# Performance work log

Measured on AMD Instinct MI355X. Metric: run time of the kernel, lower is better.

## Reference

```python
import jax, jax.numpy as jnp
import numpy as np

EPS = 1e-5
NUM_HEAD = 8
HEAD_DIM = 64
SCALE = HEAD_DIM ** -0.5


def setup_inputs() -> dict:
    key = jax.random.key(0)
    ks = jax.random.split(key, 3)
    b, n, dim = 4, 2048, 512
    inner = NUM_HEAD * HEAD_DIM  # 512
    x = jax.random.normal(ks[0], (b, n, dim), dtype=jnp.float32)
    ln_w = jnp.ones((dim,), jnp.float32)
    ln_b = jnp.zeros((dim,), jnp.float32)
    qkv_w = jax.random.normal(ks[1], (3 * inner, dim), jnp.float32) * (dim ** -0.5)
    qkv_b = jnp.zeros((3 * inner,), jnp.float32)
    out_w = jax.random.normal(ks[2], (dim, inner), jnp.float32) * (inner ** -0.5)
    out_b = jnp.zeros((dim,), jnp.float32)
    return {"x": x, "ln_w": ln_w, "ln_b": ln_b, "qkv_w": qkv_w,
            "qkv_b": qkv_b, "out_w": out_w, "out_b": out_b}


def reference(x, ln_w, ln_b, qkv_w, qkv_b, out_w, out_b):
    b, n, dim = x.shape
    # Pre-norm LayerNorm
    mu = jnp.mean(x, axis=-1, keepdims=True)
    var = jnp.mean(jnp.square(x - mu), axis=-1, keepdims=True)
    xn = (x - mu) * jax.lax.rsqrt(var + EPS) * ln_w + ln_b
    # QKV projection (torch Linear: y = x @ W.T + b)
    qkv = xn @ qkv_w.T + qkv_b  # [b, n, 3*inner]
    q, k, v = jnp.split(qkv, 3, axis=-1)
    def heads(t):  # [b, n, inner] -> [b, h, n, d]
        return t.reshape(b, n, NUM_HEAD, HEAD_DIM).transpose(0, 2, 1, 3)
    q, k, v = heads(q), heads(k), heads(v)
    # Naive full attention (materializes [b, h, n, n])
    dots = jnp.einsum('bhqd,bhkd->bhqk', q, k) * SCALE
    attn = jax.nn.softmax(dots, axis=-1)
    o = jnp.einsum('bhqk,bhkd->bhqd', attn, v)
    o = o.transpose(0, 2, 1, 3).reshape(b, n, NUM_HEAD * HEAD_DIM)
    return o @ out_w.T + out_b
```

## Files before the change

### kernel.cpp

```cpp
#include <hip/hip_runtime.h>

typedef __attribute__((ext_vector_type(8))) short bf16x8;
typedef __attribute__((ext_vector_type(4))) float floatx4;
typedef __attribute__((ext_vector_type(16))) float floatx16;
typedef __attribute__((ext_vector_type(4))) unsigned int uintx4;

#define B_    4
#define N_    2048
#define DIM_  512
#define NH_   8
#define HD_   64
#define SCALE_ 0.125f
#define SL2E_ (0.125f * 1.44269504f)

__device__ __forceinline__ unsigned short f32_to_bf16(float f) {
    return (unsigned short)((__float_as_uint(f) + 0x8000u) >> 16);
}

__device__ __forceinline__ float bf16_to_f32(unsigned short u) {
    return __uint_as_float(((unsigned int)u) << 16);
}

__device__ __forceinline__ floatx4 mfma16(bf16x8 a, bf16x8 b, floatx4 c) {
    return __builtin_amdgcn_mfma_f32_16x16x32_bf16(a, b, c, 0, 0, 0);
}

__device__ __forceinline__ floatx16 mfma32(bf16x8 a, bf16x8 b, floatx16 c) {
    return __builtin_amdgcn_mfma_f32_32x32x16_bf16(a, b, c, 0, 0, 0);
}

__device__ __forceinline__ floatx4 fzero4() {
    floatx4 z = {0.f, 0.f, 0.f, 0.f};
    return z;
}

__device__ __forceinline__ floatx16 fzero16() {
    floatx16 z;
#pragma unroll
    for (int i = 0; i < 16; i++) z[i] = 0.f;
    return z;
}

__device__ __forceinline__ unsigned int cvt_pk_bf16(float lo, float hi) {
    unsigned int r;
    asm("v_cvt_pk_bf16_f32 %0, %1, %2" : "=v"(r) : "v"(lo), "v"(hi));
    return r;
}

__device__ __forceinline__ void async16(const unsigned short* g, unsigned short* l) {
    __builtin_amdgcn_global_load_lds((const __attribute__((address_space(1))) void*)g,
                                     (__attribute__((address_space(3))) void*)l,
                                     16, 0, 0);
}

__global__ __launch_bounds__(256) void ln_kernel(const float* __restrict__ x,
                                                 const float* __restrict__ w,
                                                 const float* __restrict__ b,
                                                 unsigned short* __restrict__ xn) {
    int wv = threadIdx.x >> 6;
    int lane = threadIdx.x & 63;
    int row = blockIdx.x * 4 + wv;
    const float4* xr = (const float4*)(x + (size_t)row * DIM_);
    float4 v0 = xr[lane * 2];
    float4 v1 = xr[lane * 2 + 1];
    float s  = (v0.x + v0.y + v0.z + v0.w) + (v1.x + v1.y + v1.z + v1.w);
    float sq = v0.x*v0.x + v0.y*v0.y + v0.z*v0.z + v0.w*v0.w +
               v1.x*v1.x + v1.y*v1.y + v1.z*v1.z + v1.w*v1.w;
#pragma unroll
    for (int off = 1; off < 64; off <<= 1) {
        s  += __shfl_xor(s, off, 64);
        sq += __shfl_xor(sq, off, 64);
    }
    float mu   = s * (1.f / DIM_);
    float var  = sq * (1.f / DIM_) - mu * mu;
    float rstd = rsqrtf(var + 1e-5f);
    float4 w0 = ((const float4*)w)[lane * 2];
    float4 w1 = ((const float4*)w)[lane * 2 + 1];
    float4 b0 = ((const float4*)b)[lane * 2];
    float4 b1 = ((const float4*)b)[lane * 2 + 1];
    float y[8];
    y[0] = (v0.x - mu) * rstd * w0.x + b0.x;
    y[1] = (v0.y - mu) * rstd * w0.y + b0.y;
    y[2] = (v0.z - mu) * rstd * w0.z + b0.z;
    y[3] = (v0.w - mu) * rstd * w0.w + b0.w;
    y[4] = (v1.x - mu) * rstd * w1.x + b1.x;
    y[5] = (v1.y - mu) * rstd * w1.y + b1.y;
    y[6] = (v1.z - mu) * rstd * w1.z + b1.z;
    y[7] = (v1.w - mu) * rstd * w1.w + b1.w;
    uint4 pk;
    pk.x = (unsigned int)f32_to_bf16(y[0]) | ((unsigned int)f32_to_bf16(y[1]) << 16);
    pk.y = (unsigned int)f32_to_bf16(y[2]) | ((unsigned int)f32_to_bf16(y[3]) << 16);
    pk.z = (unsigned int)f32_to_bf16(y[4]) | ((unsigned int)f32_to_bf16(y[5]) << 16);
    pk.w = (unsigned int)f32_to_bf16(y[6]) | ((unsigned int)f32_to_bf16(y[7]) << 16);
    ((uint4*)(xn + (size_t)row * DIM_))[lane] = pk;
}

__global__ __launch_bounds__(256) void cvt_kernel(const float* __restrict__ srcA, int na,
                                                  const float* __restrict__ srcB, int nb,
                                                  unsigned short* __restrict__ dstA,
                                                  unsigned short* __restrict__ dstB) {
    int idx = blockIdx.x * 256 + threadIdx.x;
    if (idx < na)            dstA[idx] = f32_to_bf16(srcA[idx]);
    else if (idx < na + nb)  dstB[idx - na] = f32_to_bf16(srcB[idx - na]);
}

#define GEMM_CORE512(A_, B_ptr, am0, bn0)                                           \
    __shared__ unsigned short Alds[2][128][32];                                     \
    __shared__ unsigned short Blds[2][128][32];                                     \
    int tid = threadIdx.x, lane = tid & 63, wid = tid >> 6;                         \
    int l15 = lane & 15, quad = lane >> 4;                                          \
    int wmloc = (wid >> 1) * 32, wnloc = (wid & 1) * 64;                            \
    int sr = lane >> 2;                                                             \
    int sc = (lane & 3) * 8;                                                        \
    int srow0 = 16 * wid;                                                           \
    floatx4 acc[2][4];                                                              \
    _Pragma("unroll")                                                               \
    for (int i = 0; i < 2; i++)                                                     \
        _Pragma("unroll")                                                           \
        for (int j = 0; j < 4; j++) acc[i][j] = fzero4();                           \
    int buf = 0;                                                                    \
    async16(A_ + (size_t)(am0 + srow0 + sr) * DIM_ + sc, &Alds[0][srow0][0]);       \
    async16(B_ptr + (size_t)(bn0 + srow0 + sr) * DIM_ + sc, &Blds[0][srow0][0]);    \
    __syncthreads();                                                                \
    for (int t = 0; t < 16; t++) {                                                  \
        if (t < 15) {                                                               \
            int k0 = (t + 1) * 32;                                                  \
            async16(A_ + (size_t)(am0 + srow0 + sr) * DIM_ + k0 + sc,               \
                    &Alds[buf ^ 1][srow0][0]);                                      \
            async16(B_ptr + (size_t)(bn0 + srow0 + sr) * DIM_ + k0 + sc,            \
                    &Blds[buf ^ 1][srow0][0]);                                      \
        }                                                                           \
        bf16x8 av[2], bv[4];                                                        \
        _Pragma("unroll")                                                           \
        for (int i = 0; i < 2; i++)                                                 \
            av[i] = *(const bf16x8*)(&Alds[buf][wmloc + 16 * i + l15][quad * 8]);   \
        _Pragma("unroll")                                                           \
        for (int j = 0; j < 4; j++)                                                 \
            bv[j] = *(const bf16x8*)(&Blds[buf][wnloc + 16 * j + l15][quad * 8]);   \
        _Pragma("unroll")                                                           \
        for (int i = 0; i < 2; i++)                                                 \
            _Pragma("unroll")                                                       \
            for (int j = 0; j < 4; j++)                                             \
                acc[i][j] = mfma16(av[i], bv[j], acc[i][j]);                        \
        __syncthreads();                                                            \
        buf ^= 1;                                                                   \
    }

__global__ __launch_bounds__(512, 4) void qkv_gemm(const unsigned short* __restrict__ A,
                                                   const unsigned short* __restrict__ Bw,
                                                   const float* __restrict__ bias,
                                                   unsigned short* __restrict__ Qh,
                                                   unsigned short* __restrict__ Kh,
                                                   unsigned short* __restrict__ Vt) {
    int am0 = blockIdx.x * 128, bn0 = blockIdx.y * 128;
    GEMM_CORE512(A, Bw, am0, bn0)

    if (bn0 >= 1024) {
        unsigned short* sc_ = &Alds[0][0][0] + wid * (16 * 40);
        int m0 = am0 + wmloc;
        int bidx = m0 >> 11;
        int t0 = m0 & 2047;
#pragma unroll
        for (int j = 0; j < 4; j++) {
            float bias_n = bias[bn0 + wnloc + 16 * j + l15];
#pragma unroll
            for (int i = 0; i < 2; i++)
#pragma unroll
                for (int r = 0; r < 4; r++)
                    sc_[l15 * 40 + 16 * i + quad * 4 + r] =
                        f32_to_bf16(acc[i][j][r] + bias_n);
            int nr = lane >> 2;
            int rem = (bn0 - 1024) + wnloc + 16 * j + nr;
            int head = rem >> 6, d = rem & 63;
            bf16x8 vv = *(const bf16x8*)(sc_ + nr * 40 + (lane & 3) * 8);
            *(bf16x8*)(Vt + ((size_t)(bidx * NH_ + head) * HD_ + d) * N_ +
                       t0 + (lane & 3) * 8) = vv;
        }
    } else {
#pragma unroll
        for (int i = 0; i < 2; i++) {
#pragma unroll
            for (int j = 0; j < 4; j++) {
                int n = bn0 + wnloc + 16 * j + l15;
                float bias_n = bias[n];
                int which = n >> 9;
                int rem = n & 511;
                int head = rem >> 6;
                int d = rem & 63;
#pragma unroll
                for (int r = 0; r < 4; r++) {
                    int m = am0 + wmloc + 16 * i + quad * 4 + r;
                    int b = m >> 11;
                    int t = m & 2047;
                    float val = acc[i][j][r] + bias_n;
                    if (which == 0) {
                        Qh[((size_t)(b * NH_ + head) * N_ + t) * HD_ + d] =
                            f32_to_bf16(val * SL2E_);
                    } else {
                        Kh[((size_t)(b * NH_ + head) * N_ + t) * HD_ + d] =
                            f32_to_bf16(val);
                    }
                }
            }
        }
    }
}

__global__ __launch_bounds__(256, 4) void out_gemm_fused(const unsigned short* __restrict__ Opart,
                                                         const float* __restrict__ lpart,
                                                         const unsigned short* __restrict__ Bw,
                                                         const float* __restrict__ bias,
                                                         float* __restrict__ out) {
    __shared__ unsigned short Alds[2][64][36];
    __shared__ unsigned short Blds[2][128][32];
    int tid = threadIdx.x, lane = tid & 63, wid = tid >> 6;
    int l15 = lane & 15, quad = lane >> 4;
    int wmloc = (wid >> 1) * 32, wnloc = (wid & 1) * 64;
    int am0 = blockIdx.x * 64, bn0 = blockIdx.y * 128;

    int arow = tid >> 2;
    int ac8 = (tid & 3) * 8;
    int token = am0 + arow;
    int bb = token >> 11;
    const size_t LSTR = (size_t)B_ * NH_ * N_;
    const size_t OSTR = (size_t)B_ * N_ * DIM_;
    const unsigned short* arow0 = Opart + (size_t)token * DIM_;
    const unsigned short* arow1 = arow0 + OSTR;

    int sr = lane >> 2;
    int sc = (lane & 3) * 8;

    floatx4 acc[2][4];
#pragma unroll
    for (int i = 0; i < 2; i++)
#pragma unroll
        for (int j = 0; j < 4; j++) acc[i][j] = fzero4();

#define STAGE_A(BUF, T)                                                         \
    {                                                                           \
        int k0 = (T) * 32;                                                      \
        int head = k0 >> 6;                                                     \
        size_t li = (size_t)(bb * NH_ + head) * N_ + (token & 2047);            \
        float l1 = lpart[li];                                                   \
        float l2 = lpart[LSTR + li];                                            \
        float inv = 1.f / (l1 + l2);                                            \
        float w1 = l1 * inv, w2 = l2 * inv;                                     \
        bf16x8 o0 = *(const bf16x8*)(arow0 + k0 + ac8);                         \
        bf16x8 o1 = *(const bf16x8*)(arow1 + k0 + ac8);                         \
        bf16x8 pk;                                                              \
        _Pragma("unroll")                                                       \
        for (int e = 0; e < 8; e++)                                             \
            pk[e] = (short)f32_to_bf16(                                         \
                w1 * bf16_to_f32((unsigned short)o0[e]) +                       \
                w2 * bf16_to_f32((unsigned short)o1[e]));                       \
        *(bf16x8*)(&Alds[BUF][arow][ac8]) = pk;                                 \
    }

#define STAGE_B(BUF, T)                                                         \
    {                                                                           \
        int k0 = (T) * 32;                                                      \
        _Pragma("unroll")                                                       \
        for (int i = 0; i < 2; i++) {                                           \
            int r0 = 32 * wid + 16 * i;                                         \
            async16(Bw + (size_t)(bn0 + r0 + sr) * DIM_ + k0 + sc,              \
                    &Blds[BUF][r0][0]);                                         \
        }                                                                       \
    }

    STAGE_B(0, 0)
    STAGE_A(0, 0)
    __syncthreads();
    int buf = 0;
    for (int t = 0; t < 16; t++) {
        if (t < 15) {
            STAGE_B(buf ^ 1, t + 1)
            STAGE_A(buf ^ 1, t + 1)
        }
        bf16x8 av[2], bv[4];
#pragma unroll
        for (int i = 0; i < 2; i++)
            av[i] = *(const bf16x8*)(&Alds[buf][wmloc + 16 * i + l15][quad * 8]);
#pragma unroll
        for (int j = 0; j < 4; j++)
            bv[j] = *(const bf16x8*)(&Blds[buf][wnloc + 16 * j + l15][quad * 8]);
#pragma unroll
        for (int i = 0; i < 2; i++)
#pragma unroll
            for (int j = 0; j < 4; j++)
                acc[i][j] = mfma16(av[i], bv[j], acc[i][j]);
        __syncthreads();
        buf ^= 1;
    }
#undef STAGE_A
#undef STAGE_B

#pragma unroll
    for (int i = 0; i < 2; i++) {
#pragma unroll
        for (int j = 0; j < 4; j++) {
            int n = bn0 + wnloc + 16 * j + l15;
            float bias_n = bias[n];
#pragma unroll
            for (int r = 0; r < 4; r++) {
                int m = am0 + wmloc + 16 * i + quad * 4 + r;
                out[(size_t)m * DIM_ + n] = acc[i][j][r] + bias_n;
            }
        }
    }
}

__global__ __launch_bounds__(256, 4) void attn_kernel(const unsigned short* __restrict__ Qh,
                                                      const unsigned short* __restrict__ Kh,
                                                      const unsigned short* __restrict__ Vtg,
                                                      unsigned short* __restrict__ Opart,
                                                      float* __restrict__ lpart) {
    int bh = blockIdx.y;
    int b = bh >> 3, head = bh & 7;
    int qt = blockIdx.x;
    int split = blockIdx.z;
    int kv0 = split << 10;
    int tid = threadIdx.x, lane = tid & 63, w = tid >> 6;
    int l31 = lane & 31, hi = lane >> 5;
    int xr = l31 & 7;

    const unsigned short* Qp = Qh + (size_t)bh * N_ * HD_;
    const unsigned short* Kg = Kh + (size_t)bh * N_ * HD_;
    const unsigned short* Vg = Vtg + (size_t)bh * HD_ * N_;

    int q0 = qt * 128 + w * 32;

    bf16x8 aQ[4];
    {
        const unsigned short* qrow = Qp + (size_t)(q0 + l31) * HD_ + hi * 8;
#pragma unroll
        for (int t = 0; t < 4; t++)
            aQ[t] = *(const bf16x8*)(qrow + 16 * t);
    }

    __shared__ unsigned short Kt[2][64][64];
    __shared__ unsigned short Vs[2][64][64];
    __shared__ float l_sm[4][32];

    int srow = lane >> 3;
    int scol = ((lane & 7) ^ srow) * 8;

#define STAGE_KV(BUF, KV)                                                           \
    {                                                                               \
        _Pragma("unroll")                                                           \
        for (int i = 0; i < 2; i++) {                                               \
            int r0 = 16 * w + 8 * i;                                                \
            async16(Kg + (size_t)((KV) + r0 + srow) * HD_ + scol, &Kt[BUF][r0][0]); \
            async16(Vg + (size_t)(r0 + srow) * N_ + (KV) + scol, &Vs[BUF][r0][0]);  \
        }                                                                           \
    }

    STAGE_KV(0, kv0)
    __syncthreads();

    floatx16 of[2];
    of[0] = fzero16();
    of[1] = fzero16();
    float lsumA = 0.f, lsumB = 0.f;

    int buf = 0;
    for (int it = 0; it < 16; it++) {
        if (it < 15) {
            STAGE_KV(buf ^ 1, kv0 + (it + 1) * 64)
        }
        bf16x8 pa[4];
#pragma unroll
        for (int tau = 0; tau < 2; tau++) {
            bf16x8 kf[4];
#pragma unroll
            for (int t = 0; t < 4; t++)
                kf[t] = *(const bf16x8*)(&Kt[buf][32 * tau + l31][((2 * t + hi) ^ xr) * 8]);
            floatx16 acc = fzero16();
            __builtin_amdgcn_s_setprio(1);
#pragma unroll
            for (int t = 0; t < 4; t++)
                acc = mfma32(kf[t], aQ[t], acc);
            __builtin_amdgcn_s_setprio(0);
            float p[16];
#pragma unroll
            for (int r = 0; r < 16; r += 2) {
                p[r]     = exp2f(acc[r]);
                p[r + 1] = exp2f(acc[r + 1]);
                lsumA += p[r];
                lsumB += p[r + 1];
            }
            unsigned int a0 = cvt_pk_bf16(p[0], p[1]);
            unsigned int b0 = cvt_pk_bf16(p[4], p[5]);
            unsigned int a1 = cvt_pk_bf16(p[2], p[3]);
            unsigned int b1 = cvt_pk_bf16(p[6], p[7]);
            unsigned int a2 = cvt_pk_bf16(p[8], p[9]);
            unsigned int b2 = cvt_pk_bf16(p[12], p[13]);
            unsigned int a3 = cvt_pk_bf16(p[10], p[11]);
            unsigned int b3 = cvt_pk_bf16(p[14], p[15]);
            asm("v_permlane32_swap_b32 %0, %1" : "+v"(a0), "+v"(b0));
            asm("v_permlane32_swap_b32 %0, %1" : "+v"(a1), "+v"(b1));
            asm("v_permlane32_swap_b32 %0, %1" : "+v"(a2), "+v"(b2));
            asm("v_permlane32_swap_b32 %0, %1" : "+v"(a3), "+v"(b3));
            uintx4 f0 = {a0, a1, b0, b1};
            uintx4 f1 = {a2, a3, b2, b3};
            pa[2 * tau]     = __builtin_bit_cast(bf16x8, f0);
            pa[2 * tau + 1] = __builtin_bit_cast(bf16x8, f1);
        }
        __builtin_amdgcn_s_setprio(1);
#pragma unroll
        for (int s = 0; s < 4; s++) {
#pragma unroll
            for (int dt = 0; dt < 2; dt++) {
                bf16x8 vf = *(const bf16x8*)(&Vs[buf][32 * dt + l31][((2 * s + hi) ^ xr) * 8]);
                of[dt] = mfma32(pa[s], vf, of[dt]);
            }
        }
        __builtin_amdgcn_s_setprio(0);
        __syncthreads();
        buf ^= 1;
    }
#undef STAGE_KV

    float lsum = lsumA + lsumB;
    lsum += __shfl_xor(lsum, 32, 64);
    if (lane < 32) {
        l_sm[w][l31] = 1.f / lsum;
        lpart[(size_t)split * B_ * NH_ * N_ + (size_t)bh * N_ + q0 + l31] = lsum;
    }
    __syncthreads();

    unsigned short* Od = Opart + (size_t)split * B_ * N_ * DIM_;
#pragma unroll
    for (int r = 0; r < 16; r++) {
        int qr = (r & 3) + 8 * (r >> 2) + 4 * hi;
        float inv = l_sm[w][qr];
        int token = q0 + qr;
        size_t base = ((size_t)b * N_ + token) * DIM_ + (size_t)head * HD_;
#pragma unroll
        for (int dt = 0; dt < 2; dt++)
            Od[base + 32 * dt + l31] = f32_to_bf16(of[dt][r] * inv);
    }
}

extern "C" void kernel_launch(void* const* d_in, const int* in_sizes, int n_in,
                              void* d_out, int out_size, void* d_ws, size_t ws_size,
                              hipStream_t stream) {
    const float* x     = (const float*)d_in[0];
    const float* ln_w  = (const float*)d_in[1];
    const float* ln_b  = (const float*)d_in[2];
    const float* qkv_w = (const float*)d_in[3];
    const float* qkv_b = (const float*)d_in[4];
    const float* out_w = (const float*)d_in[5];
    const float* out_b = (const float*)d_in[6];
    float* out = (float*)d_out;

    char* ws = (char*)d_ws;
    const size_t TOK = (size_t)B_ * N_;
    unsigned short* xn    = (unsigned short*)ws;  ws += TOK * DIM_ * 2;
    unsigned short* wq_bf = (unsigned short*)ws;  ws += (size_t)3 * DIM_ * DIM_ * 2;
    unsigned short* wo_bf = (unsigned short*)ws;  ws += (size_t)DIM_ * DIM_ * 2;
    unsigned short* Qh    = (unsigned short*)ws;  ws += TOK * DIM_ * 2;
    unsigned short* Kh    = (unsigned short*)ws;  ws += TOK * DIM_ * 2;
    unsigned short* Vt    = (unsigned short*)ws;  ws += TOK * DIM_ * 2;
    unsigned short* Opart = (unsigned short*)ws;  ws += (size_t)2 * TOK * DIM_ * 2;
    float*          lpart = (float*)ws;           ws += (size_t)2 * B_ * NH_ * N_ * 4;

    const int NW = 3 * DIM_ * DIM_;
    const int NO = DIM_ * DIM_;

    ln_kernel<<<TOK / 4, 256, 0, stream>>>(x, ln_w, ln_b, xn);
    cvt_kernel<<<(NW + NO + 255) / 256, 256, 0, stream>>>(qkv_w, NW, out_w, NO, wq_bf, wo_bf);
    qkv_gemm<<<dim3(TOK / 128, (3 * DIM_) / 128), 512, 0, stream>>>(xn, wq_bf, qkv_b, Qh, Kh, Vt);
    attn_kernel<<<dim3(N_ / 128, B_ * NH_, 2), 256, 0, stream>>>(Qh, Kh, Vt, Opart, lpart);
    out_gemm_fused<<<dim3(TOK / 64, DIM_ / 128), 256, 0, stream>>>(Opart, lpart, wo_bf, out_b, out);
}
```

Baseline: 181.0 us.

## Compute softmax row sums with MFMA against ones and unroll double-buffered KV loop

Drops the per-element scalar accumulation of exp values and instead computes the row sums with an extra MFMA that multiplies the bf16 probability fragments by a ones vector. This removes the cross-lane shuffle, the shared-memory staging of reciprocals and one block barrier. The KV loop is manually unrolled by two with fixed buffer indices and precomputed LDS/global pointers, and exp2f is replaced by the hardware exp2 intrinsic. The row sum now comes from bf16-rounded probabilities, which slightly changes numerics, and each iteration adds four MFMAs.

```diff
diff --git a/kernel.cpp b/kernel.cpp
--- a/kernel.cpp
+++ b/kernel.cpp
@@ -337,107 +337,122 @@
             aQ[t] = *(const bf16x8*)(qrow + 16 * t);
     }
 
-    __shared__ unsigned short Kt[2][64][64];
-    __shared__ unsigned short Vs[2][64][64];
-    __shared__ float l_sm[4][32];
+    __shared__ unsigned short KV[2][2][64][64];
 
     int srow = lane >> 3;
     int scol = ((lane & 7) ^ srow) * 8;
 
-#define STAGE_KV(BUF, KV)                                                           \
-    {                                                                               \
-        _Pragma("unroll")                                                           \
-        for (int i = 0; i < 2; i++) {                                               \
-            int r0 = 16 * w + 8 * i;                                                \
-            async16(Kg + (size_t)((KV) + r0 + srow) * HD_ + scol, &Kt[BUF][r0][0]); \
-            async16(Vg + (size_t)(r0 + srow) * N_ + (KV) + scol, &Vs[BUF][r0][0]);  \
-        }                                                                           \
-    }
-
-    STAGE_KV(0, kv0)
-    __syncthreads();
+    const char* ptc[4];
+#pragma unroll
+    for (int t = 0; t < 4; t++)
+        ptc[t] = (const char*)&KV[0][0][l31][(((2 * t + hi) ^ xr) * 8)];
+
+    const unsigned short* kSrc = Kg + (size_t)(kv0 + 16 * w + srow) * HD_ + scol;
+    const unsigned short* vSrc = Vg + (size_t)(16 * w + srow) * N_ + kv0 + scol;
+
+#define STAGE_KV(BUF, IT)                                                       \
+    {                                                                           \
+        _Pragma("unroll")                                                       \
+        for (int i = 0; i < 2; i++) {                                           \
+            int r0 = 16 * w + 8 * i;                                            \
+            async16(kSrc + (size_t)(IT) * 64 * HD_ + i * 8 * HD_,               \
+                    &KV[BUF][0][r0][0]);                                        \
+            async16(vSrc + (size_t)(IT) * 64 + i * 8 * N_,                      \
+                    &KV[BUF][1][r0][0]);                                        \
+        }                                                                       \
+    }
 
     floatx16 of[2];
     of[0] = fzero16();
     of[1] = fzero16();
-    float lsumA = 0.f, lsumB = 0.f;
-
-    int buf = 0;
-    for (int it = 0; it < 16; it++) {
-        if (it < 15) {
-            STAGE_KV(buf ^ 1, kv0 + (it + 1) * 64)
-        }
-        bf16x8 pa[4];
-#pragma unroll
-        for (int tau = 0; tau < 2; tau++) {
-            bf16x8 kf[4];
-#pragma unroll
-            for (int t = 0; t < 4; t++)
-                kf[t] = *(const bf16x8*)(&Kt[buf][32 * tau + l31][((2 * t + hi) ^ xr) * 8]);
-            floatx16 acc = fzero16();
-            __builtin_amdgcn_s_setprio(1);
-#pragma unroll
-            for (int t = 0; t < 4; t++)
-                acc = mfma32(kf[t], aQ[t], acc);
-            __builtin_amdgcn_s_setprio(0);
-            float p[16];
-#pragma unroll
-            for (int r = 0; r < 16; r += 2) {
-                p[r]     = exp2f(acc[r]);
-                p[r + 1] = exp2f(acc[r + 1]);
-                lsumA += p[r];
-                lsumB += p[r + 1];
-            }
-            unsigned int a0 = cvt_pk_bf16(p[0], p[1]);
-            unsigned int b0 = cvt_pk_bf16(p[4], p[5]);
-            unsigned int a1 = cvt_pk_bf16(p[2], p[3]);
-            unsigned int b1 = cvt_pk_bf16(p[6], p[7]);
-            unsigned int a2 = cvt_pk_bf16(p[8], p[9]);
-            unsigned int b2 = cvt_pk_bf16(p[12], p[13]);
-            unsigned int a3 = cvt_pk_bf16(p[10], p[11]);
-            unsigned int b3 = cvt_pk_bf16(p[14], p[15]);
-            asm("v_permlane32_swap_b32 %0, %1" : "+v"(a0), "+v"(b0));
-            asm("v_permlane32_swap_b32 %0, %1" : "+v"(a1), "+v"(b1));
-            asm("v_permlane32_swap_b32 %0, %1" : "+v"(a2), "+v"(b2));
-            asm("v_permlane32_swap_b32 %0, %1" : "+v"(a3), "+v"(b3));
-            uintx4 f0 = {a0, a1, b0, b1};
-            uintx4 f1 = {a2, a3, b2, b3};
-            pa[2 * tau]     = __builtin_bit_cast(bf16x8, f0);
-            pa[2 * tau + 1] = __builtin_bit_cast(bf16x8, f1);
-        }
-        __builtin_amdgcn_s_setprio(1);
-#pragma unroll
-        for (int s = 0; s < 4; s++) {
-#pragma unroll
-            for (int dt = 0; dt < 2; dt++) {
-                bf16x8 vf = *(const bf16x8*)(&Vs[buf][32 * dt + l31][((2 * s + hi) ^ xr) * 8]);
-                of[dt] = mfma32(pa[s], vf, of[dt]);
-            }
-        }
-        __builtin_amdgcn_s_setprio(0);
+    floatx16 lacc = fzero16();
+
+    const short onebf = (short)0x3F80;
+    bf16x8 onesB = {onebf, onebf, onebf, onebf, onebf, onebf, onebf, onebf};
+
+#define COMPUTE(BUF)                                                            \
+    {                                                                           \
+        bf16x8 pa[4];                                                           \
+        _Pragma("unroll")                                                       \
+        for (int tau = 0; tau < 2; tau++) {                                     \
+            bf16x8 kf[4];                                                       \
+            _Pragma("unroll")                                                   \
+            for (int t = 0; t < 4; t++)                                         \
+                kf[t] = *(const bf16x8*)(ptc[t] + (BUF) * 16384 + tau * 4096);  \
+            floatx16 acc = fzero16();                                           \
+            __builtin_amdgcn_s_setprio(1);                                      \
+            _Pragma("unroll")                                                   \
+            for (int t = 0; t < 4; t++)                                         \
+                acc = mfma32(kf[t], aQ[t], acc);                                \
+            __builtin_amdgcn_s_setprio(0);                                      \
+            float p[16];                                                        \
+            _Pragma("unroll")                                                   \
+            for (int r = 0; r < 16; r++)                                        \
+                p[r] = __builtin_amdgcn_exp2f(acc[r]);                          \
+            unsigned int a0 = cvt_pk_bf16(p[0], p[1]);                          \
+            unsigned int b0 = cvt_pk_bf16(p[4], p[5]);                          \
+            unsigned int a1 = cvt_pk_bf16(p[2], p[3]);                          \
+            unsigned int b1 = cvt_pk_bf16(p[6], p[7]);                          \
+            unsigned int a2 = cvt_pk_bf16(p[8], p[9]);                          \
+            unsigned int b2 = cvt_pk_bf16(p[12], p[13]);                        \
+            unsigned int a3 = cvt_pk_bf16(p[10], p[11]);                        \
+            unsigned int b3 = cvt_pk_bf16(p[14], p[15]);                        \
+            asm("v_permlane32_swap_b32 %0, %1" : "+v"(a0), "+v"(b0));           \
+            asm("v_permlane32_swap_b32 %0, %1" : "+v"(a1), "+v"(b1));           \
+            asm("v_permlane32_swap_b32 %0, %1" : "+v"(a2), "+v"(b2));           \
+            asm("v_permlane32_swap_b32 %0, %1" : "+v"(a3), "+v"(b3));           \
+            uintx4 f0 = {a0, a1, b0, b1};                                       \
+            uintx4 f1 = {a2, a3, b2, b3};                                       \
+            pa[2 * tau]     = __builtin_bit_cast(bf16x8, f0);                   \
+            pa[2 * tau + 1] = __builtin_bit_cast(bf16x8, f1);                   \
+        }                                                                       \
+        __builtin_amdgcn_s_setprio(1);                                          \
+        _Pragma("unroll")                                                       \
+        for (int s = 0; s < 4; s++) {                                           \
+            _Pragma("unroll")                                                   \
+            for (int dt = 0; dt < 2; dt++) {                                    \
+                bf16x8 vf = *(const bf16x8*)(ptc[s] + (BUF) * 16384 + 8192 +    \
+                                             dt * 4096);                        \
+                of[dt] = mfma32(pa[s], vf, of[dt]);                             \
+            }                                                                   \
+            lacc = mfma32(pa[s], onesB, lacc);                                  \
+        }                                                                       \
+        __builtin_amdgcn_s_setprio(0);                                          \
+    }
+
+    STAGE_KV(0, 0)
+    __syncthreads();
+
+    for (int it2 = 0; it2 < 8; it2++) {
+        int it = it2 * 2;
+        STAGE_KV(1, it + 1)
+        COMPUTE(0)
         __syncthreads();
-        buf ^= 1;
+        if (it2 < 7) STAGE_KV(0, it + 2)
+        COMPUTE(1)
+        __syncthreads();
     }
 #undef STAGE_KV
-
-    float lsum = lsumA + lsumB;
-    lsum += __shfl_xor(lsum, 32, 64);
-    if (lane < 32) {
-        l_sm[w][l31] = 1.f / lsum;
-        lpart[(size_t)split * B_ * NH_ * N_ + (size_t)bh * N_ + q0 + l31] = lsum;
-    }
-    __syncthreads();
+#undef COMPUTE
 
     unsigned short* Od = Opart + (size_t)split * B_ * N_ * DIM_;
 #pragma unroll
     for (int r = 0; r < 16; r++) {
         int qr = (r & 3) + 8 * (r >> 2) + 4 * hi;
-        float inv = l_sm[w][qr];
+        float inv = __builtin_amdgcn_rcpf(lacc[r]);
         int token = q0 + qr;
         size_t base = ((size_t)b * N_ + token) * DIM_ + (size_t)head * HD_;
 #pragma unroll
         for (int dt = 0; dt < 2; dt++)
             Od[base + 32 * dt + l31] = f32_to_bf16(of[dt][r] * inv);
+    }
+    if (l31 == 0) {
+#pragma unroll
+        for (int r = 0; r < 16; r++) {
+            int qr = (r & 3) + 8 * (r >> 2) + 4 * hi;
+            lpart[(size_t)split * B_ * NH_ * N_ + (size_t)bh * N_ + q0 + qr] =
+                lacc[r];
+        }
     }
 }
 
```

New measurement: 161.2 us. 1.12x faster.
